# Optimization experiments

Hardware: AMD Instinct MI355X
Metric: run time of the kernel (lower is better)

Reference implementation:

```python
import jax, jax.numpy as jnp
import numpy as np

N = 100000
E = 1600000
D = 128

def _degrees(idx, n):
    d = jax.ops.segment_sum(jnp.ones(idx.shape[0], jnp.float32), idx, num_segments=n)
    return jnp.clip(d, 1.0)

def _gconv(feat, src, dst, W, b, residual, act):
    n = feat.shape[0]
    norm_out = _degrees(src, n) ** -0.5            # [N] out-degree norm
    h = feat * norm_out[:, None]                   # scale src features
    msgs = h[src]                                  # gather [E, D]
    agg = jax.ops.segment_sum(msgs, dst, num_segments=n)  # scatter-sum [N, D]
    rst = agg @ W.T + b                            # dense linear
    norm_in = _degrees(dst, n) ** -0.5             # [N] in-degree norm
    rst = rst * norm_in[:, None]
    if residual:
        rst = rst + feat                           # identity residual (in==out)
    if act:
        rst = jax.nn.relu(rst)
    return rst

def setup_inputs() -> dict:
    key = jax.random.key(0)
    ks = jax.random.split(key, 10)
    feat = jax.random.normal(ks[0], (N, D), jnp.float32)
    src = jax.random.randint(ks[1], (E,), 0, N)
    dst = jax.random.randint(ks[2], (E,), 0, N)
    s = 1.0 / np.sqrt(D)
    W1 = jax.random.uniform(ks[3], (D, D), jnp.float32, -s, s)
    b1 = jax.random.uniform(ks[4], (D,), jnp.float32, -s, s)
    W2 = jax.random.uniform(ks[5], (D, D), jnp.float32, -s, s)
    b2 = jax.random.uniform(ks[6], (D,), jnp.float32, -s, s)
    W3 = jax.random.uniform(ks[7], (D, D), jnp.float32, -s, s)
    b3 = jax.random.uniform(ks[8], (D,), jnp.float32, -s, s)
    return {"feat": feat, "src": src, "dst": dst,
            "W1": W1, "b1": b1, "W2": W2, "b2": b2, "W3": W3, "b3": b3}

def reference(feat, src, dst, W1, b1, W2, b2, W3, b3):
    # 3-layer GCN, dropout=0, norm=None, encoding=False:
    # layers 0,1: residual + relu; layer 2: no residual, no activation
    h = _gconv(feat, src, dst, W1, b1, residual=True, act=True)
    h = _gconv(h, src, dst, W2, b2, residual=True, act=True)
    h = _gconv(h, src, dst, W3, b3, residual=False, act=False)
    return h
```

## Files before the change

kernel.cpp:

```cpp
#include <hip/hip_runtime.h>

#define NN 100000
#define EE 1600000
#define DD 128
#define NB 512
#define CAP 4608
#define CHUNK 8192

typedef __attribute__((ext_vector_type(8))) short short8v;
typedef __attribute__((ext_vector_type(4))) float f32x4;
typedef __attribute__((ext_vector_type(8))) unsigned short ushort8v;

#define LROW 136

static __device__ __forceinline__ unsigned short f2bf(float x) {
  unsigned u = __builtin_bit_cast(unsigned, x);
  return (unsigned short)((u + 0x7FFFu + ((u >> 16) & 1u)) >> 16);
}
static __device__ __forceinline__ float bf2f(unsigned short u) {
  return __builtin_bit_cast(float, (unsigned)u << 16);
}

__global__ __launch_bounds__(512) void initcur_k(int* __restrict__ cur_d,
                                                 int* __restrict__ cur_s) {
  int t = threadIdx.x;
  cur_d[t] = t * CAP;
  cur_s[t] = t * CAP;
}

__global__ __launch_bounds__(256) void split_k(const int* __restrict__ src,
                                               const int* __restrict__ dst,
                                               int* __restrict__ cur_d,
                                               int* __restrict__ cur_s,
                                               unsigned* __restrict__ tmp_d,
                                               unsigned char* __restrict__ tmp_s) {
  __shared__ int hd[NB], hs[NB], bd[NB], bs[NB];
  int t = threadIdx.x;
  int base = blockIdx.x * CHUNK;
  int end = base + CHUNK < EE ? base + CHUNK : EE;
  for (int b = t; b < NB; b += 256) { hd[b] = 0; hs[b] = 0; }
  __syncthreads();
  for (int i = base + t; i < end; i += 256) {
    atomicAdd(&hd[dst[i] >> 8], 1);
    atomicAdd(&hs[src[i] >> 8], 1);
  }
  __syncthreads();
  for (int b = t; b < NB; b += 256) {
    bd[b] = hd[b] ? atomicAdd(&cur_d[b], hd[b]) : 0;
    bs[b] = hs[b] ? atomicAdd(&cur_s[b], hs[b]) : 0;
    hd[b] = 0;
    hs[b] = 0;
  }
  __syncthreads();
  for (int i = base + t; i < end; i += 256) {
    int s = src[i];
    int d = dst[i];
    int bin = d >> 8;
    int r = atomicAdd(&hd[bin], 1);
    int pos = bd[bin] + r;
    if (pos < (bin + 1) * CAP) tmp_d[pos] = ((unsigned)(d & 255) << 17) | (unsigned)s;
    bin = s >> 8;
    r = atomicAdd(&hs[bin], 1);
    pos = bs[bin] + r;
    if (pos < (bin + 1) * CAP) tmp_s[pos] = (unsigned char)(s & 255);
  }
}

__global__ __launch_bounds__(256) void bucket_both_k(const unsigned* __restrict__ tmp_d,
                                                     const unsigned char* __restrict__ tmp_s,
                                                     const int* __restrict__ cur_d,
                                                     const int* __restrict__ cur_s,
                                                     int* __restrict__ csr,
                                                     int* __restrict__ row_s,
                                                     int* __restrict__ row_e,
                                                     float* __restrict__ norm_in,
                                                     float* __restrict__ norm_out) {
  __shared__ unsigned stage[CAP];
  __shared__ int h[256], sc[256], rk[256], h2[256];
  int b = blockIdx.x;
  int t = threadIdx.x;
  int cnt = cur_d[b] - b * CAP;
  cnt = cnt < CAP ? cnt : CAP;
  int cnts = cur_s[b] - b * CAP;
  cnts = cnts < CAP ? cnts : CAP;
  for (int i = t; i < cnt; i += 256) stage[i] = tmp_d[b * CAP + i];
  h[t] = 0;
  h2[t] = 0;
  __syncthreads();
  const unsigned char* p = tmp_s + b * CAP;
  for (int i = t; i < cnts; i += 256) atomicAdd(&h2[p[i]], 1);
  for (int i = t; i < cnt; i += 256) atomicAdd(&h[stage[i] >> 17], 1);
  __syncthreads();
  int v = h[t];
  sc[t] = v;
  __syncthreads();
  int run = v;
  for (int off = 1; off < 256; off <<= 1) {
    int y = (t >= off) ? sc[t - off] : 0;
    __syncthreads();
    run += y;
    sc[t] = run;
    __syncthreads();
  }
  int excl = run - v;
  int n = b * 256 + t;
  if (n < NN) {
    row_s[n] = b * CAP + excl;
    row_e[n] = b * CAP + excl + v;
    norm_in[n] = rsqrtf((float)(v > 1 ? v : 1));
    norm_out[n] = rsqrtf((float)(h2[t] > 1 ? h2[t] : 1));
  }
  rk[t] = excl;
  __syncthreads();
  for (int i = t; i < cnt; i += 256) {
    unsigned w = stage[i];
    int r = atomicAdd(&rk[w >> 17], 1);
    csr[b * CAP + r] = (int)(w & 0x1FFFFu);
  }
}

__global__ __launch_bounds__(256) void conv_all_k(const float* __restrict__ W1,
                                                  const float* __restrict__ W2,
                                                  const float* __restrict__ W3,
                                                  const float* __restrict__ feat,
                                                  unsigned short* __restrict__ Wbf,
                                                  unsigned short* __restrict__ vb1) {
  int b = blockIdx.x;
  const float* srcp;
  unsigned short* dstp;
  int idx;
  if (b < 16)      { srcp = W1;   dstp = Wbf;         idx = b; }
  else if (b < 32) { srcp = W2;   dstp = Wbf + 16384; idx = b - 16; }
  else if (b < 48) { srcp = W3;   dstp = Wbf + 32768; idx = b - 32; }
  else             { srcp = feat; dstp = vb1;         idx = b - 48; }
  int i = idx * 256 + threadIdx.x;
  float4 v = *reinterpret_cast<const float4*>(srcp + i * 4);
  ushort4 pk = make_ushort4(f2bf(v.x), f2bf(v.y), f2bf(v.z), f2bf(v.w));
  *reinterpret_cast<ushort4*>(dstp + i * 4) = pk;
}

__global__ __launch_bounds__(256) void layer_k(const unsigned short* __restrict__ h,
                                               const int* __restrict__ csr,
                                               const int* __restrict__ row_s,
                                               const int* __restrict__ row_e,
                                               const float* __restrict__ nsrc,
                                               const unsigned short* __restrict__ Wb,
                                               const float* __restrict__ bias,
                                               const float* __restrict__ nin,
                                               const float* __restrict__ residf,
                                               const unsigned short* __restrict__ residb,
                                               float* __restrict__ outf,
                                               unsigned short* __restrict__ outb,
                                               int mode) {
  __shared__ unsigned short tile[16 * LROW];
  int t = threadIdx.x;
  int n16 = t >> 4;
  int c = t & 15;
  int node = blockIdx.x * 16 + n16;

  int e0 = row_s[node];
  int e1 = row_e[node];
  float acc[8] = {0.f, 0.f, 0.f, 0.f, 0.f, 0.f, 0.f, 0.f};
  const unsigned short* hb = h + c * 8;
  int e = e0;
  for (; e + 4 <= e1; e += 4) {
    int s0 = csr[e];
    int s1 = csr[e + 1];
    int s2 = csr[e + 2];
    int s3 = csr[e + 3];
    float n0 = nsrc[s0];
    float n1 = nsrc[s1];
    float n2 = nsrc[s2];
    float n3 = nsrc[s3];
    ushort8v u0 = *reinterpret_cast<const ushort8v*>(hb + (size_t)s0 * DD);
    ushort8v u1 = *reinterpret_cast<const ushort8v*>(hb + (size_t)s1 * DD);
    ushort8v u2 = *reinterpret_cast<const ushort8v*>(hb + (size_t)s2 * DD);
    ushort8v u3 = *reinterpret_cast<const ushort8v*>(hb + (size_t)s3 * DD);
#pragma unroll
    for (int i = 0; i < 8; ++i) {
      acc[i] += bf2f(u0[i]) * n0 + bf2f(u1[i]) * n1 +
                bf2f(u2[i]) * n2 + bf2f(u3[i]) * n3;
    }
  }
  for (; e < e1; ++e) {
    int s0 = csr[e];
    float n0 = nsrc[s0];
    ushort8v u = *reinterpret_cast<const ushort8v*>(hb + (size_t)s0 * DD);
#pragma unroll
    for (int i = 0; i < 8; ++i) acc[i] += bf2f(u[i]) * n0;
  }
  ushort8v o;
#pragma unroll
  for (int i = 0; i < 8; ++i) o[i] = f2bf(acc[i]);
  *reinterpret_cast<ushort8v*>(&tile[n16 * LROW + c * 8]) = o;
  __syncthreads();

  int wid = t >> 6;
  int lane = t & 63;
  int l15 = lane & 15;
  int kgrp = lane >> 4;

  const unsigned short* bp = &tile[l15 * LROW + kgrp * 8];
  short8v b0 = *reinterpret_cast<const short8v*>(bp);
  short8v b1 = *reinterpret_cast<const short8v*>(bp + 32);
  short8v b2 = *reinterpret_cast<const short8v*>(bp + 64);
  short8v b3 = *reinterpret_cast<const short8v*>(bp + 96);

  int epnode = blockIdx.x * 16 + l15;
  float ninv = nin[epnode];

#pragma unroll
  for (int q = 0; q < 2; ++q) {
    int ct = wid * 2 + q;
    const unsigned short* wp = Wb + (size_t)(ct * 16 + l15) * DD + kgrp * 8;
    short8v w0 = *reinterpret_cast<const short8v*>(wp);
    short8v w1 = *reinterpret_cast<const short8v*>(wp + 32);
    short8v w2 = *reinterpret_cast<const short8v*>(wp + 64);
    short8v w3 = *reinterpret_cast<const short8v*>(wp + 96);
    f32x4 cacc = {0.f, 0.f, 0.f, 0.f};
    cacc = __builtin_amdgcn_mfma_f32_16x16x32_bf16(w0, b0, cacc, 0, 0, 0);
    cacc = __builtin_amdgcn_mfma_f32_16x16x32_bf16(w1, b1, cacc, 0, 0, 0);
    cacc = __builtin_amdgcn_mfma_f32_16x16x32_bf16(w2, b2, cacc, 0, 0, 0);
    cacc = __builtin_amdgcn_mfma_f32_16x16x32_bf16(w3, b3, cacc, 0, 0, 0);

    int j = ct * 16 + kgrp * 4;
    float4 bj = *reinterpret_cast<const float4*>(bias + j);
    size_t idx = (size_t)epnode * DD + j;
    float4 v;
    v.x = (cacc[0] + bj.x) * ninv;
    v.y = (cacc[1] + bj.y) * ninv;
    v.z = (cacc[2] + bj.z) * ninv;
    v.w = (cacc[3] + bj.w) * ninv;
    if (mode == 1) {
      float4 rs = *reinterpret_cast<const float4*>(residf + idx);
      v.x = fmaxf(v.x + rs.x, 0.f);
      v.y = fmaxf(v.y + rs.y, 0.f);
      v.z = fmaxf(v.z + rs.z, 0.f);
      v.w = fmaxf(v.w + rs.w, 0.f);
      ushort4 hn = make_ushort4(f2bf(v.x), f2bf(v.y), f2bf(v.z), f2bf(v.w));
      *reinterpret_cast<ushort4*>(outb + idx) = hn;
    } else if (mode == 3) {
      ushort4 rs = *reinterpret_cast<const ushort4*>(residb + idx);
      v.x = fmaxf(v.x + bf2f(rs.x), 0.f);
      v.y = fmaxf(v.y + bf2f(rs.y), 0.f);
      v.z = fmaxf(v.z + bf2f(rs.z), 0.f);
      v.w = fmaxf(v.w + bf2f(rs.w), 0.f);
      ushort4 hn = make_ushort4(f2bf(v.x), f2bf(v.y), f2bf(v.z), f2bf(v.w));
      *reinterpret_cast<ushort4*>(outb + idx) = hn;
    } else {
      *reinterpret_cast<float4*>(outf + idx) = v;
    }
  }
}

extern "C" void kernel_launch(void* const* d_in, const int* in_sizes, int n_in,
                              void* d_out, int out_size, void* d_ws, size_t ws_size,
                              hipStream_t stream) {
  const float* feat = (const float*)d_in[0];
  const int* src = (const int*)d_in[1];
  const int* dst = (const int*)d_in[2];
  const float* W1 = (const float*)d_in[3];
  const float* b1 = (const float*)d_in[4];
  const float* W2 = (const float*)d_in[5];
  const float* b2 = (const float*)d_in[6];
  const float* W3 = (const float*)d_in[7];
  const float* b3 = (const float*)d_in[8];
  float* out = (float*)d_out;

  int* row_s = (int*)d_ws;
  int* row_e = row_s + NN;
  float* norm_out = (float*)(row_e + NN);
  float* norm_in = norm_out + NN;
  int* cur_d = (int*)(norm_in + NN);
  int* cur_s = cur_d + NB;
  int* pad = cur_s + NB;
  unsigned short* Wbf = (unsigned short*)pad;
  int* csr = (int*)(Wbf + 3 * 16384);
  unsigned short* vb1 = (unsigned short*)(csr + NB * CAP);
  unsigned short* vb2 = vb1 + (size_t)NN * DD;

  unsigned* tmp_d = (unsigned*)d_out;
  unsigned char* tmp_s = (unsigned char*)d_out + (size_t)NB * CAP * 4;

  initcur_k<<<1, 512, 0, stream>>>(cur_d, cur_s);
  split_k<<<(EE + CHUNK - 1) / CHUNK, 256, 0, stream>>>(src, dst, cur_d, cur_s, tmp_d, tmp_s);
  bucket_both_k<<<NB, 256, 0, stream>>>(tmp_d, tmp_s, cur_d, cur_s, csr, row_s, row_e,
                                        norm_in, norm_out);
  conv_all_k<<<48 + 12500, 256, 0, stream>>>(W1, W2, W3, feat, Wbf, vb1);

  layer_k<<<6250, 256, 0, stream>>>(vb1, csr, row_s, row_e, norm_out, Wbf, b1,
                                    norm_in, feat, nullptr, nullptr, vb2, 1);
  layer_k<<<6250, 256, 0, stream>>>(vb2, csr, row_s, row_e, norm_out, Wbf + 16384, b2,
                                    norm_in, nullptr, vb2, nullptr, vb1, 3);
  layer_k<<<6250, 256, 0, stream>>>(vb1, csr, row_s, row_e, norm_out, Wbf + 32768, b3,
                                    norm_in, nullptr, nullptr, out, nullptr, 0);
}
```

Baseline: 316.3 us.

## Sort nodes by in-degree within buckets and fuse conversion into split kernel

Builds a per-bucket permutation of nodes ordered by in-degree (capped at 63) so each 16-node block in the layer kernel handles nodes of similar degree, reducing intra-block imbalance in the gather loop. The fp32-to-bf16 conversion of weights and features is also merged into the edge-split kernel launch, removing one launch and letting the two run concurrently. The trade-off is an extra perm indirection in every layer block, and epilogue residual and output accesses now follow the permuted node order, which scatters them.

Result: slower. 340.3 us (+7.6%).

```diff
diff --git a/kernel.cpp b/kernel.cpp
--- a/kernel.cpp
+++ b/kernel.cpp
@@ -6,6 +6,7 @@
 #define NB 512
 #define CAP 4608
 #define CHUNK 8192
+#define SPLITB 196
 
 typedef __attribute__((ext_vector_type(8))) short short8v;
 typedef __attribute__((ext_vector_type(4))) float f32x4;
@@ -28,14 +29,37 @@
   cur_s[t] = t * CAP;
 }
 
-__global__ __launch_bounds__(256) void split_k(const int* __restrict__ src,
-                                               const int* __restrict__ dst,
-                                               int* __restrict__ cur_d,
-                                               int* __restrict__ cur_s,
-                                               unsigned* __restrict__ tmp_d,
-                                               unsigned char* __restrict__ tmp_s) {
+__global__ __launch_bounds__(256) void split_conv_k(const int* __restrict__ src,
+                                                    const int* __restrict__ dst,
+                                                    int* __restrict__ cur_d,
+                                                    int* __restrict__ cur_s,
+                                                    unsigned* __restrict__ tmp_d,
+                                                    unsigned char* __restrict__ tmp_s,
+                                                    const float* __restrict__ W1,
+                                                    const float* __restrict__ W2,
+                                                    const float* __restrict__ W3,
+                                                    const float* __restrict__ feat,
+                                                    unsigned short* __restrict__ Wbf,
+                                                    unsigned short* __restrict__ vb1) {
   __shared__ int hd[NB], hs[NB], bd[NB], bs[NB];
   int t = threadIdx.x;
+
+  if (blockIdx.x >= SPLITB) {
+    int b = blockIdx.x - SPLITB;
+    const float* srcp;
+    unsigned short* dstp;
+    int idx;
+    if (b < 16)      { srcp = W1;   dstp = Wbf;         idx = b; }
+    else if (b < 32) { srcp = W2;   dstp = Wbf + 16384; idx = b - 16; }
+    else if (b < 48) { srcp = W3;   dstp = Wbf + 32768; idx = b - 32; }
+    else             { srcp = feat; dstp = vb1;         idx = b - 48; }
+    int i = idx * 256 + t;
+    float4 v = *reinterpret_cast<const float4*>(srcp + i * 4);
+    ushort4 pk = make_ushort4(f2bf(v.x), f2bf(v.y), f2bf(v.z), f2bf(v.w));
+    *reinterpret_cast<ushort4*>(dstp + i * 4) = pk;
+    return;
+  }
+
   int base = blockIdx.x * CHUNK;
   int end = base + CHUNK < EE ? base + CHUNK : EE;
   for (int b = t; b < NB; b += 256) { hd[b] = 0; hs[b] = 0; }
@@ -74,9 +98,11 @@
                                                      int* __restrict__ row_s,
                                                      int* __restrict__ row_e,
                                                      float* __restrict__ norm_in,
-                                                     float* __restrict__ norm_out) {
+                                                     float* __restrict__ norm_out,
+                                                     int* __restrict__ perm) {
   __shared__ unsigned stage[CAP];
   __shared__ int h[256], sc[256], rk[256], h2[256];
+  __shared__ int dh[64], dsc[64], drk[64];
   int b = blockIdx.x;
   int t = threadIdx.x;
   int cnt = cur_d[b] - b * CAP;
@@ -86,6 +112,7 @@
   for (int i = t; i < cnt; i += 256) stage[i] = tmp_d[b * CAP + i];
   h[t] = 0;
   h2[t] = 0;
+  if (t < 64) { dh[t] = 0; drk[t] = 0; }
   __syncthreads();
   const unsigned char* p = tmp_s + b * CAP;
   for (int i = t; i < cnts; i += 256) atomicAdd(&h2[p[i]], 1);
@@ -104,45 +131,43 @@
   }
   int excl = run - v;
   int n = b * 256 + t;
-  if (n < NN) {
+  bool valid = n < NN;
+  if (valid) {
     row_s[n] = b * CAP + excl;
     row_e[n] = b * CAP + excl + v;
     norm_in[n] = rsqrtf((float)(v > 1 ? v : 1));
     norm_out[n] = rsqrtf((float)(h2[t] > 1 ? h2[t] : 1));
   }
   rk[t] = excl;
+  int dbin = v > 63 ? 63 : v;
+  if (valid) atomicAdd(&dh[dbin], 1);
   __syncthreads();
   for (int i = t; i < cnt; i += 256) {
     unsigned w = stage[i];
     int r = atomicAdd(&rk[w >> 17], 1);
     csr[b * CAP + r] = (int)(w & 0x1FFFFu);
   }
-}
-
-__global__ __launch_bounds__(256) void conv_all_k(const float* __restrict__ W1,
-                                                  const float* __restrict__ W2,
-                                                  const float* __restrict__ W3,
-                                                  const float* __restrict__ feat,
-                                                  unsigned short* __restrict__ Wbf,
-                                                  unsigned short* __restrict__ vb1) {
-  int b = blockIdx.x;
-  const float* srcp;
-  unsigned short* dstp;
-  int idx;
-  if (b < 16)      { srcp = W1;   dstp = Wbf;         idx = b; }
-  else if (b < 32) { srcp = W2;   dstp = Wbf + 16384; idx = b - 16; }
-  else if (b < 48) { srcp = W3;   dstp = Wbf + 32768; idx = b - 32; }
-  else             { srcp = feat; dstp = vb1;         idx = b - 48; }
-  int i = idx * 256 + threadIdx.x;
-  float4 v = *reinterpret_cast<const float4*>(srcp + i * 4);
-  ushort4 pk = make_ushort4(f2bf(v.x), f2bf(v.y), f2bf(v.z), f2bf(v.w));
-  *reinterpret_cast<ushort4*>(dstp + i * 4) = pk;
+  if (t < 64) {
+    int val = dh[t];
+    int rn = val;
+    for (int off = 1; off < 64; off <<= 1) {
+      int y = __shfl_up(rn, off, 64);
+      if (t >= off) rn += y;
+    }
+    dsc[t] = rn - val;
+  }
+  __syncthreads();
+  if (valid) {
+    int r = atomicAdd(&drk[dbin], 1);
+    perm[b * 256 + dsc[dbin] + r] = n;
+  }
 }
 
 __global__ __launch_bounds__(256) void layer_k(const unsigned short* __restrict__ h,
                                                const int* __restrict__ csr,
                                                const int* __restrict__ row_s,
                                                const int* __restrict__ row_e,
+                                               const int* __restrict__ perm,
                                                const float* __restrict__ nsrc,
                                                const unsigned short* __restrict__ Wb,
                                                const float* __restrict__ bias,
@@ -156,7 +181,8 @@
   int t = threadIdx.x;
   int n16 = t >> 4;
   int c = t & 15;
-  int node = blockIdx.x * 16 + n16;
+  int bb = blockIdx.x * 16;
+  int node = perm[bb + n16];
 
   int e0 = row_s[node];
   int e1 = row_e[node];
@@ -206,7 +232,7 @@
   short8v b2 = *reinterpret_cast<const short8v*>(bp + 64);
   short8v b3 = *reinterpret_cast<const short8v*>(bp + 96);
 
-  int epnode = blockIdx.x * 16 + l15;
+  int epnode = perm[bb + l15];
   float ninv = nin[epnode];
 
 #pragma unroll
@@ -271,7 +297,8 @@
   int* row_e = row_s + NN;
   float* norm_out = (float*)(row_e + NN);
   float* norm_in = norm_out + NN;
-  int* cur_d = (int*)(norm_in + NN);
+  int* perm = (int*)(norm_in + NN);
+  int* cur_d = perm + NN;
   int* cur_s = cur_d + NB;
   int* pad = cur_s + NB;
   unsigned short* Wbf = (unsigned short*)pad;
@@ -283,15 +310,15 @@
   unsigned char* tmp_s = (unsigned char*)d_out + (size_t)NB * CAP * 4;
 
   initcur_k<<<1, 512, 0, stream>>>(cur_d, cur_s);
-  split_k<<<(EE + CHUNK - 1) / CHUNK, 256, 0, stream>>>(src, dst, cur_d, cur_s, tmp_d, tmp_s);
+  split_conv_k<<<SPLITB + 48 + 12500, 256, 0, stream>>>(src, dst, cur_d, cur_s, tmp_d,
+                                                        tmp_s, W1, W2, W3, feat, Wbf, vb1);
   bucket_both_k<<<NB, 256, 0, stream>>>(tmp_d, tmp_s, cur_d, cur_s, csr, row_s, row_e,
-                                        norm_in, norm_out);
-  conv_all_k<<<48 + 12500, 256, 0, stream>>>(W1, W2, W3, feat, Wbf, vb1);
-
-  layer_k<<<6250, 256, 0, stream>>>(vb1, csr, row_s, row_e, norm_out, Wbf, b1,
+                                        norm_in, norm_out, perm);
+
+  layer_k<<<6250, 256, 0, stream>>>(vb1, csr, row_s, row_e, perm, norm_out, Wbf, b1,
                                     norm_in, feat, nullptr, nullptr, vb2, 1);
-  layer_k<<<6250, 256, 0, stream>>>(vb2, csr, row_s, row_e, norm_out, Wbf + 16384, b2,
+  layer_k<<<6250, 256, 0, stream>>>(vb2, csr, row_s, row_e, perm, norm_out, Wbf + 16384, b2,
                                     norm_in, nullptr, vb2, nullptr, vb1, 3);
-  layer_k<<<6250, 256, 0, stream>>>(vb1, csr, row_s, row_e, norm_out, Wbf + 32768, b3,
+  layer_k<<<6250, 256, 0, stream>>>(vb1, csr, row_s, row_e, perm, norm_out, Wbf + 32768, b3,
                                     norm_in, nullptr, nullptr, out, nullptr, 0);
 }
```
